# Performance work log

Measured on AMD Instinct MI355X. Metric: run time of the kernel, lower is better.

The kernel has to match this reference:

```python
import jax, jax.numpy as jnp
import numpy as np

N = 100000      # nodes
E = 320000      # edges
G = 2048        # graphs
NODE_F, EDGE_F, HID, EDGE_DIM, L = 48, 6, 256, 128, 8


def setup_inputs() -> dict:
    key = jax.random.key(0)
    ks = jax.random.split(key, 16)
    s = 0.05
    return dict(
        x=jax.random.normal(ks[0], (N, NODE_F), jnp.float32),
        edge_attr=jax.random.normal(ks[1], (E, EDGE_F), jnp.float32),
        node_w=jax.random.normal(ks[2], (NODE_F, HID), jnp.float32) * s,
        node_b=jnp.zeros((HID,), jnp.float32),
        edge_w=jax.random.normal(ks[3], (EDGE_F, EDGE_DIM), jnp.float32) * s,
        edge_b=jnp.zeros((EDGE_DIM,), jnp.float32),
        conv_edge_w=jax.random.normal(ks[4], (L, EDGE_DIM, HID), jnp.float32) * s,
        conv_edge_b=jnp.zeros((L, HID), jnp.float32),
        mlp_w1=jax.random.normal(ks[5], (L, HID, HID), jnp.float32) * s,
        mlp_b1=jnp.zeros((L, HID), jnp.float32),
        mlp_w2=jax.random.normal(ks[6], (L, HID, HID), jnp.float32) * s,
        mlp_b2=jnp.zeros((L, HID), jnp.float32),
        eps=jnp.zeros((L,), jnp.float32),  # GINE trainable eps, init 0
        bn_gamma=jnp.ones((L, HID), jnp.float32),
        bn_beta=jnp.zeros((L, HID), jnp.float32),
        att_w1=jax.random.normal(ks[7], (HID, HID // 2), jnp.float32) * s,
        att_b1=jnp.zeros((HID // 2,), jnp.float32),
        att_w2=jax.random.normal(ks[8], (HID // 2, 1), jnp.float32) * s,
        att_b2=jnp.zeros((1,), jnp.float32),
        edge_index=jax.random.randint(ks[9], (2, E), 0, N),
        batch=jnp.sort(jax.random.randint(ks[10], (N,), 0, G)),
        num_graphs=G,
    )


def reference(x, edge_attr, node_w, node_b, edge_w, edge_b, conv_edge_w, conv_edge_b,
              mlp_w1, mlp_b1, mlp_w2, mlp_b2, eps, bn_gamma, bn_beta,
              att_w1, att_b1, att_w2, att_b2, edge_index, batch, num_graphs):
    seg_sum = lambda v, ids, n: jax.ops.segment_sum(v, ids, num_segments=n)
    n_nodes = x.shape[0]
    src, dst = edge_index[0], edge_index[1]  # x_j gathered from src, aggregated at dst

    h = x @ node_w + node_b                      # node embedding [N, HID]
    e = edge_attr @ edge_w + edge_b              # edge embedding [E, EDGE_DIM]
    cnt = jnp.maximum(seg_sum(jnp.ones((n_nodes,), h.dtype), batch, num_graphs), 1.0)

    for i in range(conv_edge_w.shape[0]):
        # GINEConv: msg = ReLU(x_j + Lin(edge_emb)); add-aggregate; MLP((1+eps)x + agg)
        ee = e @ conv_edge_w[i] + conv_edge_b[i]             # [E, HID]
        msg = jax.nn.relu(h[src] + ee)
        agg = seg_sum(msg, dst, n_nodes)
        z = (1.0 + eps[i]) * h + agg
        z = jax.nn.relu(z @ mlp_w1[i] + mlp_b1[i]) @ mlp_w2[i] + mlp_b2[i]
        # BatchNorm1d (batch statistics, biased var, eps=1e-5)
        mu = z.mean(0)
        var = z.var(0)
        z = bn_gamma[i] * (z - mu) * jax.lax.rsqrt(var + 1e-5) + bn_beta[i]
        # PairNorm (per-graph center, then normalize by sqrt(eps + mean sq norm))
        gmean = seg_sum(z, batch, num_graphs) / cnt[:, None]
        z = z - gmean[batch]
        msq = seg_sum(jnp.sum(z * z, axis=-1), batch, num_graphs) / cnt
        z = z * jax.lax.rsqrt(1e-5 + msq)[batch][:, None]
        h = jax.nn.relu(z)

    # pooling: mean + max + attention (exp-score softmax per graph)
    mean_pool = seg_sum(h, batch, num_graphs) / cnt[:, None]
    max_pool = jax.ops.segment_max(h, batch, num_segments=num_graphs)
    max_pool = jnp.where(jnp.isfinite(max_pool), max_pool, 0.0)
    scores = jnp.tanh(h @ att_w1 + att_b1) @ att_w2 + att_b2   # [N, 1]
    w = jnp.exp(scores)
    w = w / (seg_sum(w, batch, num_graphs)[batch] + 1e-8)
    att_pool = seg_sum(h * w, batch, num_graphs)
    return jnp.concatenate([mean_pool, max_pool, att_pool], axis=-1)  # [G, 768]
```

## Files before the change

### kernel.cpp

```cpp
#include <hip/hip_runtime.h>
#include <cstdint>
#include <cstddef>

#define NN 100000
#define EE 320000
#define GG 2048
#define LL 8

#define O_Z    0ull
#define O_ZB   25600000ull
#define O_HB   38400000ull
#define O_S1   51200000ull
#define O_S2   (O_S1 + 524288ull)
#define O_ABUF (O_S2 + 524288ull)
#define O_BBUF (O_ABUF + 256ull)
#define O_CNTI (O_BBUF + 256ull)
#define O_CNTF (O_CNTI + 2048ull)
#define O_SCOR (O_CNTF + 2048ull)
#define O_WEFF (O_SCOR + 100000ull)
#define O_BEFF (O_WEFF + 12288ull)
#define O_DEG  (O_BEFF + 2048ull)
#define O_STRT (O_DEG + 100000ull)
#define O_BSUM (O_STRT + 100000ull)
#define O_CSR  (O_BSUM + 512ull)
#define O_W1P  (O_CSR + 1280000ull)
#define O_W2P  (O_W1P + 262144ull)
#define O_ATP  (O_W2P + 262144ull)
#define O_GST  (O_ATP + 16384ull)
#define O_NWP  (O_GST + 2048ull)

typedef short s16x8 __attribute__((ext_vector_type(8)));
typedef float f32x4 __attribute__((ext_vector_type(4)));

__device__ inline float b2f(unsigned int lo16) {
  union { float f; unsigned int u; } x; x.u = lo16 << 16; return x.f;
}
__device__ inline unsigned short f2b(float f) {
  union { float f; unsigned int u; } x; x.f = f;
  unsigned int r = x.u + 0x7FFFu + ((x.u >> 16) & 1u);
  return (unsigned short)(r >> 16);
}
__device__ inline unsigned short f2b_lo(float v) {
  unsigned short h = f2b(v);
  float hf = b2f((unsigned int)h);
  return f2b(v - hf);
}

__global__ __launch_bounds__(256) void k_zero(float* __restrict__ p, int n) {
  int i = blockIdx.x * 256 + threadIdx.x;
  int stride = gridDim.x * 256;
  for (; i < n; i += stride) p[i] = 0.0f;
}

__global__ __launch_bounds__(256) void k_count(const int* __restrict__ batch, int* __restrict__ cnti, int n) {
  int i = blockIdx.x * 256 + threadIdx.x;
  if (i < n) atomicAdd(&cnti[batch[i]], 1);
}

__global__ __launch_bounds__(256) void k_gscan(const int* __restrict__ cnti, int* __restrict__ gstart,
                                               float* __restrict__ cntf) {
  __shared__ int part[256];
  int t = threadIdx.x;
  int base = t * 8;
  int loc[8];
  int s = 0;
#pragma unroll
  for (int i = 0; i < 8; ++i) { loc[i] = s; s += cnti[base + i]; }
  part[t] = s;
  __syncthreads();
  for (int off = 1; off < 256; off <<= 1) {
    int u = (t >= off) ? part[t - off] : 0;
    __syncthreads();
    part[t] += u;
    __syncthreads();
  }
  int p = (t > 0) ? part[t - 1] : 0;
#pragma unroll
  for (int i = 0; i < 8; ++i) {
    gstart[base + i] = p + loc[i];
    float v = (float)cnti[base + i];
    cntf[base + i] = v > 1.0f ? v : 1.0f;
  }
}

__global__ __launch_bounds__(256) void k_deg(const int* __restrict__ edst, int* __restrict__ deg, int ne) {
  int e = blockIdx.x * 256 + threadIdx.x;
  if (e < ne) atomicAdd(&deg[edst[e]], 1);
}

__global__ __launch_bounds__(256) void k_scan_part(const int* __restrict__ deg, int* __restrict__ start,
                                                   int* __restrict__ bsum, int n) {
  __shared__ int s[256];
  int i = blockIdx.x * 256 + threadIdx.x;
  int t = threadIdx.x;
  int v = (i < n) ? deg[i] : 0;
  s[t] = v;
  __syncthreads();
  for (int off = 1; off < 256; off <<= 1) {
    int u = (t >= off) ? s[t - off] : 0;
    __syncthreads();
    s[t] += u;
    __syncthreads();
  }
  if (i < n) start[i] = s[t] - v;
  if (t == 255) bsum[blockIdx.x] = s[255];
}

__global__ __launch_bounds__(512) void k_scan_top(int* __restrict__ bsum, int nb) {
  __shared__ int s[512];
  int t = threadIdx.x;
  int v = (t < nb) ? bsum[t] : 0;
  s[t] = v;
  __syncthreads();
  for (int off = 1; off < 512; off <<= 1) {
    int u = (t >= off) ? s[t - off] : 0;
    __syncthreads();
    s[t] += u;
    __syncthreads();
  }
  if (t < nb) bsum[t] = s[t] - v;
}

__global__ __launch_bounds__(256) void k_scan_add(int* __restrict__ start, const int* __restrict__ bsum,
                                                  int* __restrict__ cursor, int n) {
  int i = blockIdx.x * 256 + threadIdx.x;
  if (i < n) {
    int v = start[i] + bsum[blockIdx.x];
    start[i] = v;
    cursor[i] = v;
  }
}

__global__ __launch_bounds__(256) void k_fill(const float* __restrict__ ea, const int* __restrict__ esrc,
                                              const int* __restrict__ edst, int* __restrict__ cursor,
                                              uint4* __restrict__ csr, int ne) {
  int e = blockIdx.x * 256 + threadIdx.x;
  if (e >= ne) return;
  int d = edst[e];
  int slot = atomicAdd(&cursor[d], 1);
  const float* ap = ea + (size_t)e * 6;
  uint4 v;
  v.x = (unsigned int)f2b(ap[0]) | ((unsigned int)f2b(ap[1]) << 16);
  v.y = (unsigned int)f2b(ap[2]) | ((unsigned int)f2b(ap[3]) << 16);
  v.z = (unsigned int)f2b(ap[4]) | ((unsigned int)f2b(ap[5]) << 16);
  v.w = (unsigned int)esrc[e];
  csr[slot] = v;
}

__global__ __launch_bounds__(256) void k_wfuse(const float* __restrict__ edge_w, const float* __restrict__ edge_b,
                                               const float* __restrict__ conv_w, const float* __restrict__ conv_b,
                                               float* __restrict__ wef, float* __restrict__ bef) {
  __shared__ float ew[6 * 128 + 128];
  int i = blockIdx.x;
  int c = threadIdx.x;
  for (int idx = c; idx < 896; idx += 256)
    ew[idx] = idx < 768 ? edge_w[idx] : edge_b[idx - 768];
  __syncthreads();
  float acc[7] = {0.f, 0.f, 0.f, 0.f, 0.f, 0.f, 0.f};
  const float* cw = conv_w + (size_t)i * 32768 + c;
  for (int j = 0; j < 128; ++j) {
    float w = cw[(size_t)j * 256];
#pragma unroll
    for (int k = 0; k < 6; ++k) acc[k] = fmaf(ew[k * 128 + j], w, acc[k]);
    acc[6] = fmaf(ew[768 + j], w, acc[6]);
  }
#pragma unroll
  for (int k = 0; k < 6; ++k) wef[(size_t)i * 1536 + k * 256 + c] = acc[k];
  bef[(size_t)i * 256 + c] = acc[6] + conv_b[(size_t)i * 256 + c];
}

__global__ __launch_bounds__(256) void k_pack_all(const float* __restrict__ mw1, const float* __restrict__ mw2,
                                                  const float* __restrict__ aw1,
                                                  unsigned short* __restrict__ w1p,
                                                  unsigned short* __restrict__ w2p,
                                                  unsigned short* __restrict__ atp) {
  int id = blockIdx.x * 256 + threadIdx.x;
  int cbu = id >> 12;
  if (cbu >= 33) return;
  int lid = id & 4095;
  int l = lid & 63;
  int ct = (lid >> 6) & 7;
  int ks = (lid >> 9) & 7;
  const float* B;
  unsigned short* Bp;
  int ldb, cb;
  if (cbu < 32) {
    int m = cbu >> 1;
    cb = cbu & 1;
    ldb = 256;
    if (m < 8) { B = mw1 + (size_t)m * 65536; Bp = w1p + (size_t)m * 65536; }
    else       { B = mw2 + (size_t)(m - 8) * 65536; Bp = w2p + (size_t)(m - 8) * 65536; }
  } else {
    B = aw1; Bp = atp; ldb = 128; cb = 0;
  }
  int n = cb * 128 + ct * 16 + (l & 15);
  int k0 = ks * 32 + (l >> 4) * 8;
  unsigned short* dst = Bp + (((size_t)cb << 12) | (size_t)lid) * 8;
#pragma unroll
  for (int j = 0; j < 8; ++j) dst[j] = f2b(B[(size_t)(k0 + j) * ldb + n]);
}

__global__ __launch_bounds__(256) void k_pack_node(const float* __restrict__ w,
                                                   unsigned short* __restrict__ Wp) {
  int id = blockIdx.x * 256 + threadIdx.x;
  if (id >= 3072) return;
  int l = id & 63;
  int t = id >> 6;
  int ct = t & 7;
  int u = t >> 3;
  int ks = u % 3;
  int cb = u / 3;
  int n = cb * 128 + ct * 16 + (l & 15);
  unsigned short* dst = Wp + (size_t)id * 8;
#pragma unroll
  for (int j = 0; j < 8; ++j) {
    int kk = ks * 32 + ((l >> 4) << 3) + j;
    int ksrc = kk < 48 ? kk : kk - 48;
    dst[j] = f2b(w[(size_t)ksrc * 256 + n]);
  }
}

__global__ __launch_bounds__(256) void k_embed_mfma(const float* __restrict__ x,
                                                    const unsigned short* __restrict__ Wp,
                                                    const float* __restrict__ b,
                                                    unsigned short* __restrict__ hb, int M) {
  int l = threadIdx.x & 63;
  int w = threadIdx.x >> 6;
  int mloc = l & 15, q = l >> 4;
  int row0 = blockIdx.x * 64 + (w & 1) * 32;
  int colh = (w >> 1) * 128;

  f32x4 acc[2][8];
#pragma unroll
  for (int rt = 0; rt < 2; ++rt)
#pragma unroll
    for (int ct = 0; ct < 8; ++ct) acc[rt][ct] = (f32x4){0.f, 0.f, 0.f, 0.f};

  union { s16x8 v; unsigned short u[8]; } a[2][3];
#pragma unroll
  for (int rt = 0; rt < 2; ++rt) {
    int r = row0 + rt * 16 + mloc;
    if (r > M - 1) r = M - 1;
    const float* xr = x + (size_t)r * 48;
    const float* p0 = xr + q * 8;
    const float* p1 = xr + (q < 2 ? 32 + q * 8 : (q - 2) * 8);
    const float* p2 = xr + 16 + q * 8;
#pragma unroll
    for (int j = 0; j < 8; ++j) {
      a[rt][0].u[j] = f2b(p0[j]);
      a[rt][1].u[j] = (q < 2) ? f2b(p1[j]) : f2b_lo(p1[j]);
      a[rt][2].u[j] = f2b_lo(p2[j]);
    }
  }

  const unsigned short* bp = Wp + (size_t)(colh >> 7) * 12288 + (size_t)l * 8;
#pragma unroll
  for (int ks = 0; ks < 3; ++ks) {
#pragma unroll
    for (int ct = 0; ct < 8; ++ct) {
      s16x8 bb = *(const s16x8*)(bp + ks * 4096 + ct * 512);
      acc[0][ct] = __builtin_amdgcn_mfma_f32_16x16x32_bf16(a[0][ks].v, bb, acc[0][ct], 0, 0, 0);
      acc[1][ct] = __builtin_amdgcn_mfma_f32_16x16x32_bf16(a[1][ks].v, bb, acc[1][ct], 0, 0, 0);
    }
  }

#pragma unroll
  for (int ct = 0; ct < 8; ++ct) {
    int col = colh + ct * 16 + mloc;
    float bv = b[col];
#pragma unroll
    for (int rt = 0; rt < 2; ++rt)
#pragma unroll
      for (int r = 0; r < 4; ++r) {
        int row = row0 + rt * 16 + q * 4 + r;
        if (row < M) hb[(size_t)row * 256 + col] = f2b(acc[rt][ct][r] + bv);
      }
  }
}

__global__ __launch_bounds__(256) void k_edge_csr(const uint4* __restrict__ csr,
                                                  const int* __restrict__ startv, const int* __restrict__ degv,
                                                  const float* __restrict__ wef, const float* __restrict__ bef,
                                                  const unsigned short* __restrict__ hb,
                                                  unsigned short* __restrict__ zb,
                                                  const float* __restrict__ eps, int layer, int n) {
  int lane = threadIdx.x & 63;
  int wv = threadIdx.x >> 6;
  int v0 = (blockIdx.x * 4 + wv) * 4;
  if (v0 >= n) return;
  int c0 = lane * 4;
  float4 w0 = *(const float4*)(wef + 0 * 256 + c0);
  float4 w1 = *(const float4*)(wef + 1 * 256 + c0);
  float4 w2 = *(const float4*)(wef + 2 * 256 + c0);
  float4 w3 = *(const float4*)(wef + 3 * 256 + c0);
  float4 w4 = *(const float4*)(wef + 4 * 256 + c0);
  float4 w5 = *(const float4*)(wef + 5 * 256 + c0);
  float4 bf = *(const float4*)(bef + c0);
  float s = 1.0f + eps[layer];

  int dg[4], pp[4];
  float4 acc[4];
#pragma unroll
  for (int k = 0; k < 4; ++k) {
    int v = v0 + k;
    dg[k] = degv[v];
    int st = startv[v];
    pp[k] = st < (EE - 1) ? st : (EE - 1);
    uint2 hu = *(const uint2*)(hb + (size_t)v * 256 + c0);
    acc[k].x = s * b2f(hu.x & 0xFFFFu);
    acc[k].y = s * b2f(hu.x >> 16);
    acc[k].z = s * b2f(hu.y & 0xFFFFu);
    acc[k].w = s * b2f(hu.y >> 16);
  }
  int mx = dg[0] > dg[1] ? dg[0] : dg[1];
  int mx2 = dg[2] > dg[3] ? dg[2] : dg[3];
  if (mx2 > mx) mx = mx2;

  for (int t = 0; t < mx; ++t) {
    uint4 e[4];
#pragma unroll
    for (int k = 0; k < 4; ++k) e[k] = csr[pp[k]];
    uint2 g[4];
#pragma unroll
    for (int k = 0; k < 4; ++k) g[k] = *(const uint2*)(hb + (size_t)(int)e[k].w * 256 + c0);
#pragma unroll
    for (int k = 0; k < 4; ++k) {
      if (t < dg[k]) {
        float a0 = b2f(e[k].x & 0xFFFFu), a1 = b2f(e[k].x >> 16), a2 = b2f(e[k].y & 0xFFFFu);
        float a3 = b2f(e[k].y >> 16), a4 = b2f(e[k].z & 0xFFFFu), a5 = b2f(e[k].z >> 16);
        float mxv = fmaf(a0, w0.x, fmaf(a1, w1.x, fmaf(a2, w2.x, fmaf(a3, w3.x, fmaf(a4, w4.x, fmaf(a5, w5.x, b2f(g[k].x & 0xFFFFu) + bf.x))))));
        float myv = fmaf(a0, w0.y, fmaf(a1, w1.y, fmaf(a2, w2.y, fmaf(a3, w3.y, fmaf(a4, w4.y, fmaf(a5, w5.y, b2f(g[k].x >> 16) + bf.y))))));
        float mzv = fmaf(a0, w0.z, fmaf(a1, w1.z, fmaf(a2, w2.z, fmaf(a3, w3.z, fmaf(a4, w4.z, fmaf(a5, w5.z, b2f(g[k].y & 0xFFFFu) + bf.z))))));
        float mwv = fmaf(a0, w0.w, fmaf(a1, w1.w, fmaf(a2, w2.w, fmaf(a3, w3.w, fmaf(a4, w4.w, fmaf(a5, w5.w, b2f(g[k].y >> 16) + bf.w))))));
        acc[k].x += mxv > 0.f ? mxv : 0.f;
        acc[k].y += myv > 0.f ? myv : 0.f;
        acc[k].z += mzv > 0.f ? mzv : 0.f;
        acc[k].w += mwv > 0.f ? mwv : 0.f;
      }
      pp[k] += (t < dg[k] - 1) ? 1 : 0;
    }
  }
#pragma unroll
  for (int k = 0; k < 4; ++k) {
    uint2 o;
    o.x = (unsigned int)f2b(acc[k].x) | ((unsigned int)f2b(acc[k].y) << 16);
    o.y = (unsigned int)f2b(acc[k].z) | ((unsigned int)f2b(acc[k].w) << 16);
    *(uint2*)(zb + (size_t)(v0 + k) * 256 + c0) = o;
  }
}

__global__ __launch_bounds__(256, 4) void k_mlp(const unsigned short* __restrict__ A,
                                                const unsigned short* __restrict__ W1p,
                                                const float* __restrict__ b1,
                                                const unsigned short* __restrict__ W2p,
                                                const float* __restrict__ b2,
                                                float* __restrict__ Z,
                                                const int* __restrict__ batchv,
                                                float* __restrict__ S1, float* __restrict__ S2, int M) {
  __shared__ __align__(16) unsigned char smem[33024];
  unsigned short* t1s = (unsigned short*)smem;
  float* zc = (float*)smem;
  int l = threadIdx.x & 63;
  int w = threadIdx.x >> 6;
  int mloc = l & 15, q = l >> 4;
  int rowg = (w & 1) * 32;
  int colh = (w >> 1) * 128;
  int row0 = blockIdx.x * 64;

  const unsigned short* ap[2];
#pragma unroll
  for (int rt = 0; rt < 2; ++rt) {
    int r = row0 + rowg + rt * 16 + mloc;
    if (r > M - 1) r = M - 1;
    ap[rt] = A + (size_t)r * 256 + q * 8;
  }
  f32x4 acc[2][8];
#pragma unroll
  for (int rt = 0; rt < 2; ++rt)
#pragma unroll
    for (int ct = 0; ct < 8; ++ct) acc[rt][ct] = (f32x4){0.f, 0.f, 0.f, 0.f};

  const unsigned short* w1base = W1p + ((size_t)(colh >> 7)) * 32768 + (size_t)l * 8;
#pragma unroll
  for (int ks = 0; ks < 8; ++ks) {
    s16x8 a0 = *(const s16x8*)(ap[0] + ks * 32);
    s16x8 a1 = *(const s16x8*)(ap[1] + ks * 32);
#pragma unroll
    for (int ct = 0; ct < 8; ++ct) {
      s16x8 b = *(const s16x8*)(w1base + ks * 4096 + ct * 512);
      acc[0][ct] = __builtin_amdgcn_mfma_f32_16x16x32_bf16(a0, b, acc[0][ct], 0, 0, 0);
      acc[1][ct] = __builtin_amdgcn_mfma_f32_16x16x32_bf16(a1, b, acc[1][ct], 0, 0, 0);
    }
  }
#pragma unroll
  for (int ct = 0; ct < 8; ++ct) {
    int col = colh + ct * 16 + mloc;
    float bv = b1[col];
    int cc = col >> 3, pos = col & 7;
#pragma unroll
    for (int rt = 0; rt < 2; ++rt)
#pragma unroll
      for (int r = 0; r < 4; ++r) {
        int row = rowg + rt * 16 + q * 4 + r;
        float v = acc[rt][ct][r] + bv;
        v = v > 0.f ? v : 0.f;
        t1s[row * 256 + ((cc ^ (row & 31)) << 3) + pos] = f2b(v);
      }
  }
  __syncthreads();
#pragma unroll
  for (int rt = 0; rt < 2; ++rt)
#pragma unroll
    for (int ct = 0; ct < 8; ++ct) acc[rt][ct] = (f32x4){0.f, 0.f, 0.f, 0.f};
  const unsigned short* w2base = W2p + ((size_t)(colh >> 7)) * 32768 + (size_t)l * 8;
#pragma unroll
  for (int ks = 0; ks < 8; ++ks) {
    s16x8 a[2];
#pragma unroll
    for (int rt = 0; rt < 2; ++rt) {
      int row = rowg + rt * 16 + mloc;
      int cc = (q + ks * 4) ^ (row & 31);
      a[rt] = *(const s16x8*)(t1s + row * 256 + (cc << 3));
    }
#pragma unroll
    for (int ct = 0; ct < 8; ++ct) {
      s16x8 b = *(const s16x8*)(w2base + ks * 4096 + ct * 512);
      acc[0][ct] = __builtin_amdgcn_mfma_f32_16x16x32_bf16(a[0], b, acc[0][ct], 0, 0, 0);
      acc[1][ct] = __builtin_amdgcn_mfma_f32_16x16x32_bf16(a[1], b, acc[1][ct], 0, 0, 0);
    }
  }
  float bv2[8];
#pragma unroll
  for (int ct = 0; ct < 8; ++ct) bv2[ct] = b2[colh + ct * 16 + mloc];

#pragma unroll
  for (int half = 0; half < 2; ++half) {
    __syncthreads();
    if ((w & 1) == half) {
#pragma unroll
      for (int ct = 0; ct < 8; ++ct) {
        int col = colh + ct * 16 + mloc;
#pragma unroll
        for (int rt = 0; rt < 2; ++rt)
#pragma unroll
          for (int r = 0; r < 4; ++r) {
            int row = rt * 16 + q * 4 + r;
            zc[row * 258 + col] = acc[rt][ct][r] + bv2[ct];
          }
      }
    }
    __syncthreads();
    int baserow = row0 + half * 32;
#pragma unroll
    for (int it = 0; it < 8; ++it) {
      int row = it * 4 + w;
      int grow = baserow + row;
      float4 vv = *(const float4*)(zc + row * 258 + l * 4);
      if (grow < M) *(float4*)(Z + (size_t)grow * 256 + l * 4) = vv;
    }
    {
      int c = threadIdx.x;
      int rend = (M - baserow) < 32 ? (M - baserow) : 32;
      if (rend > 0) {
        float s1 = 0.f, s2 = 0.f;
        int gcur = batchv[baserow];
        for (int row = 0; row < rend; ++row) {
          int g = batchv[baserow + row];
          if (g != gcur) {
            atomicAdd(&S1[(size_t)gcur * 256 + c], s1);
            atomicAdd(&S2[(size_t)gcur * 256 + c], s2);
            s1 = 0.f; s2 = 0.f; gcur = g;
          }
          float v = zc[row * 258 + c];
          s1 += v;
          s2 = fmaf(v, v, s2);
        }
        atomicAdd(&S1[(size_t)gcur * 256 + c], s1);
        atomicAdd(&S2[(size_t)gcur * 256 + c], s2);
      }
    }
  }
}

__global__ __launch_bounds__(256) void k_att(const unsigned short* __restrict__ A,
                                             const unsigned short* __restrict__ Bp,
                                             const float* __restrict__ b1,
                                             const float* __restrict__ w2,
                                             const float* __restrict__ b2,
                                             float* __restrict__ scores, int M) {
  int l = threadIdx.x & 63;
  int w = threadIdx.x >> 6;
  int mloc = l & 15, q = l >> 4;
  int row0 = blockIdx.x * 128 + w * 32;

  int r0 = row0 + mloc;      if (r0 > M - 1) r0 = M - 1;
  int r1 = row0 + 16 + mloc; if (r1 > M - 1) r1 = M - 1;
  const unsigned short* ap0 = A + (size_t)r0 * 256 + q * 8;
  const unsigned short* ap1 = A + (size_t)r1 * 256 + q * 8;
  const unsigned short* bp = Bp + (size_t)l * 8;

  f32x4 acc[2][8];
#pragma unroll
  for (int rt = 0; rt < 2; ++rt)
#pragma unroll
    for (int ct = 0; ct < 8; ++ct) acc[rt][ct] = (f32x4){0.f, 0.f, 0.f, 0.f};
#pragma unroll
  for (int ks = 0; ks < 8; ++ks) {
    s16x8 a0 = *(const s16x8*)(ap0 + ks * 32);
    s16x8 a1 = *(const s16x8*)(ap1 + ks * 32);
#pragma unroll
    for (int ct = 0; ct < 8; ++ct) {
      s16x8 b = *(const s16x8*)(bp + ks * 4096 + ct * 512);
      acc[0][ct] = __builtin_amdgcn_mfma_f32_16x16x32_bf16(a0, b, acc[0][ct], 0, 0, 0);
      acc[1][ct] = __builtin_amdgcn_mfma_f32_16x16x32_bf16(a1, b, acc[1][ct], 0, 0, 0);
    }
  }
  float bv[8], wv[8];
#pragma unroll
  for (int ct = 0; ct < 8; ++ct) {
    bv[ct] = b1[ct * 16 + mloc];
    wv[ct] = w2[ct * 16 + mloc];
  }
  float b2v = b2[0];
#pragma unroll
  for (int rt = 0; rt < 2; ++rt)
#pragma unroll
    for (int r = 0; r < 4; ++r) {
      float p = 0.0f;
#pragma unroll
      for (int ct = 0; ct < 8; ++ct) p = fmaf(tanhf(acc[rt][ct][r] + bv[ct]), wv[ct], p);
      p += __shfl_xor(p, 1, 64);
      p += __shfl_xor(p, 2, 64);
      p += __shfl_xor(p, 4, 64);
      p += __shfl_xor(p, 8, 64);
      int row = row0 + rt * 16 + q * 4 + r;
      if (mloc == 0 && row < M) scores[row] = p + b2v;
    }
}

__global__ __launch_bounds__(256) void k_bn_fin(const float* __restrict__ S1, const float* __restrict__ S2,
                                                const float* __restrict__ gamma, const float* __restrict__ beta,
                                                float* __restrict__ abuf, float* __restrict__ bbuf, int n) {
  __shared__ float r1[256], r2[256];
  int c = blockIdx.x;
  int t = threadIdx.x;
  float s1 = 0.0f, s2 = 0.0f;
  for (int g = t; g < GG; g += 256) {
    s1 += S1[(size_t)g * 256 + c];
    s2 += S2[(size_t)g * 256 + c];
  }
  r1[t] = s1; r2[t] = s2;
  __syncthreads();
  for (int off = 128; off; off >>= 1) {
    if (t < off) { r1[t] += r1[t + off]; r2[t] += r2[t + off]; }
    __syncthreads();
  }
  if (t == 0) {
    float inv = 1.0f / (float)n;
    float mu = r1[0] * inv;
    float var = r2[0] * inv - mu * mu;
    float rstd = rsqrtf(var + 1e-5f);
    float a = gamma[c] * rstd;
    abuf[c] = a;
    bbuf[c] = beta[c] - mu * a;
  }
}

template <int LAST>
__global__ __launch_bounds__(256) void k_apply(float* __restrict__ z, const float* __restrict__ abuf,
                                               const float* __restrict__ bbuf, const int* __restrict__ gstart,
                                               const int* __restrict__ cnti, const float* __restrict__ cntf,
                                               float* __restrict__ S1, float* __restrict__ S2,
                                               unsigned short* __restrict__ hb) {
  __shared__ float rT[256], rM[256];
  int g = blockIdx.x, c = threadIdx.x;
  float a = abuf[c], b = bbuf[c];
  size_t idx = (size_t)g * 256 + c;
  float s1 = S1[idx];
  float s2 = S2[idx];
  S1[idx] = 0.0f;
  S2[idx] = 0.0f;
  float nr = (float)cnti[g];
  float ic = 1.0f / cntf[g];
  float mean = (a * s1 + nr * b) * ic;
  float term = fmaf(a * a, s2, fmaf(2.0f * a * b, s1, nr * b * b));
  rT[c] = term;
  rM[c] = mean * mean;
  __syncthreads();
  for (int off = 128; off; off >>= 1) {
    if (c < off) { rT[c] += rT[c + off]; rM[c] += rM[c + off]; }
    __syncthreads();
  }
  float cr = nr > 0.0f ? 1.0f : 0.0f;
  float rinv = rsqrtf(1e-5f + rT[0] * ic - cr * rM[0]);
  int r0 = gstart[g], r1 = r0 + cnti[g];
  for (int r = r0; r < r1; ++r) {
    float v = (fmaf(a, z[(size_t)r * 256 + c], b) - mean) * rinv;
    v = v > 0.0f ? v : 0.0f;
    hb[(size_t)r * 256 + c] = f2b(v);
    if (LAST) z[(size_t)r * 256 + c] = v;
  }
}

__global__ __launch_bounds__(256) void k_poolout(const float* __restrict__ h, const float* __restrict__ scores,
                                                 const int* __restrict__ gstart, const int* __restrict__ cnti,
                                                 const float* __restrict__ cntf, float* __restrict__ out) {
  int g = blockIdx.x, c = threadIdx.x;
  int r0 = gstart[g], r1 = r0 + cnti[g];
  float ma = 0.0f, aa = 0.0f, mx = 0.0f, wa = 0.0f;
  for (int r = r0; r < r1; ++r) {
    float wgt = __expf(scores[r]);
    float hv = h[(size_t)r * 256 + c];
    ma += hv;
    aa = fmaf(hv, wgt, aa);
    mx = fmaxf(mx, hv);
    wa += wgt;
  }
  out[(size_t)g * 768 + c] = ma / cntf[g];
  out[(size_t)g * 768 + 256 + c] = mx;
  out[(size_t)g * 768 + 512 + c] = aa / (wa + 1e-8f);
}

extern "C" void kernel_launch(void* const* d_in, const int* in_sizes, int n_in,
                              void* d_out, int out_size, void* d_ws, size_t ws_size,
                              hipStream_t stream) {
  const float* x         = (const float*)d_in[0];
  const float* edge_attr = (const float*)d_in[1];
  const float* node_w    = (const float*)d_in[2];
  const float* node_b    = (const float*)d_in[3];
  const float* edge_w    = (const float*)d_in[4];
  const float* edge_b    = (const float*)d_in[5];
  const float* conv_w    = (const float*)d_in[6];
  const float* conv_b    = (const float*)d_in[7];
  const float* mlp_w1    = (const float*)d_in[8];
  const float* mlp_b1    = (const float*)d_in[9];
  const float* mlp_w2    = (const float*)d_in[10];
  const float* mlp_b2    = (const float*)d_in[11];
  const float* eps       = (const float*)d_in[12];
  const float* bn_gamma  = (const float*)d_in[13];
  const float* bn_beta   = (const float*)d_in[14];
  const float* att_w1    = (const float*)d_in[15];
  const float* att_b1    = (const float*)d_in[16];
  const float* att_w2    = (const float*)d_in[17];
  const float* att_b2    = (const float*)d_in[18];
  const int*   eidx      = (const int*)d_in[19];
  const int*   batch     = (const int*)d_in[20];
  float* out = (float*)d_out;
  float* ws  = (float*)d_ws;

  float*          zbuf = ws + O_Z;
  unsigned short* zb   = (unsigned short*)(ws + O_ZB);
  unsigned short* hb   = (unsigned short*)(ws + O_HB);
  float* S1    = ws + O_S1;
  float* S2    = ws + O_S2;
  float* abuf  = ws + O_ABUF;
  float* bbuf  = ws + O_BBUF;
  int*   cnti  = (int*)(ws + O_CNTI);
  float* cntf  = ws + O_CNTF;
  float* scor  = ws + O_SCOR;
  int*   curs  = (int*)(ws + O_SCOR);
  float* weff  = ws + O_WEFF;
  float* beff  = ws + O_BEFF;
  int*   deg   = (int*)(ws + O_DEG);
  int*   strt  = (int*)(ws + O_STRT);
  int*   bsum  = (int*)(ws + O_BSUM);
  uint4* csr   = (uint4*)(ws + O_CSR);
  unsigned short* w1p = (unsigned short*)(ws + O_W1P);
  unsigned short* w2p = (unsigned short*)(ws + O_W2P);
  unsigned short* atp = (unsigned short*)(ws + O_ATP);
  int*   gst   = (int*)(ws + O_GST);
  unsigned short* nwp = (unsigned short*)(ws + O_NWP);
  const int* esrc = eidx;
  const int* edst = eidx + EE;

  k_zero<<<8, 256, 0, stream>>>((float*)cnti, GG);
  k_count<<<(NN + 255) / 256, 256, 0, stream>>>(batch, cnti, NN);
  k_gscan<<<1, 256, 0, stream>>>(cnti, gst, cntf);

  k_wfuse<<<LL, 256, 0, stream>>>(edge_w, edge_b, conv_w, conv_b, weff, beff);
  k_pack_all<<<528, 256, 0, stream>>>(mlp_w1, mlp_w2, att_w1, w1p, w2p, atp);
  k_pack_node<<<12, 256, 0, stream>>>(node_w, nwp);
  k_embed_mfma<<<(NN + 63) / 64, 256, 0, stream>>>(x, nwp, node_b, hb, NN);

  k_zero<<<1024, 256, 0, stream>>>(S1, 2 * 524288);

  const int nscan = (NN + 255) / 256;
  k_zero<<<256, 256, 0, stream>>>((float*)deg, NN);
  k_deg<<<(EE + 255) / 256, 256, 0, stream>>>(edst, deg, EE);
  k_scan_part<<<nscan, 256, 0, stream>>>(deg, strt, bsum, NN);
  k_scan_top<<<1, 512, 0, stream>>>(bsum, nscan);
  k_scan_add<<<nscan, 256, 0, stream>>>(strt, bsum, curs, NN);
  k_fill<<<(EE + 255) / 256, 256, 0, stream>>>(edge_attr, esrc, edst, curs, csr, EE);

  const int mtiles64  = (NN + 63) / 64;
  const int mtiles128 = (NN + 127) / 128;

  for (int i = 0; i < LL; ++i) {
    k_edge_csr<<<NN / 16, 256, 0, stream>>>(csr, strt, deg, weff + (size_t)i * 1536,
                                            beff + (size_t)i * 256, hb, zb, eps, i, NN);
    k_mlp<<<mtiles64, 256, 0, stream>>>(zb, w1p + (size_t)i * 65536, mlp_b1 + (size_t)i * 256,
                                        w2p + (size_t)i * 65536, mlp_b2 + (size_t)i * 256, zbuf,
                                        batch, S1, S2, NN);
    k_bn_fin<<<256, 256, 0, stream>>>(S1, S2, bn_gamma + (size_t)i * 256, bn_beta + (size_t)i * 256,
                                      abuf, bbuf, NN);
    if (i == LL - 1)
      k_apply<1><<<GG, 256, 0, stream>>>(zbuf, abuf, bbuf, gst, cnti, cntf, S1, S2, hb);
    else
      k_apply<0><<<GG, 256, 0, stream>>>(zbuf, abuf, bbuf, gst, cnti, cntf, S1, S2, hb);
  }

  k_att<<<mtiles128, 256, 0, stream>>>(hb, atp, att_b1, att_w2, att_b2, scor, NN);
  k_poolout<<<GG, 256, 0, stream>>>(zbuf, scor, gst, cnti, cntf, out);
}
```

Before: 1.705 ms.

## Stage embed inputs in LDS, prefetch CSR entries, split BN reduction

The node-embedding kernel now loads its 64x48 input tile into shared memory with coalesced loads, so threads no longer read strided rows from global memory. The edge aggregation loop prefetches the next CSR entry while the current neighbor gather is in flight, which shortens the dependent load chain. The BatchNorm finalize step, which ran 256 blocks each striding across 2048 rows of a single column, becomes a two-stage reduction: 64 blocks read coalesced partial sums and one block combines them. This adds a kernel launch per layer and a small partial buffer in the workspace.

```diff
diff --git a/kernel.cpp b/kernel.cpp
--- a/kernel.cpp
+++ b/kernel.cpp
@@ -28,6 +28,7 @@
 #define O_ATP  (O_W2P + 262144ull)
 #define O_GST  (O_ATP + 16384ull)
 #define O_NWP  (O_GST + 2048ull)
+#define O_BNP  (O_NWP + 12288ull)
 
 typedef short s16x8 __attribute__((ext_vector_type(8)));
 typedef float f32x4 __attribute__((ext_vector_type(4)));
@@ -224,10 +225,20 @@
                                                     const unsigned short* __restrict__ Wp,
                                                     const float* __restrict__ b,
                                                     unsigned short* __restrict__ hb, int M) {
-  int l = threadIdx.x & 63;
-  int w = threadIdx.x >> 6;
+  __shared__ float xs[64 * 50];
+  int tid = threadIdx.x;
+  int row0g = blockIdx.x * 64;
+  for (int idx = tid; idx < 3072; idx += 256) {
+    int r = idx / 48, c = idx - r * 48;
+    int gr = row0g + r; if (gr > M - 1) gr = M - 1;
+    xs[r * 50 + c] = x[(size_t)gr * 48 + c];
+  }
+  __syncthreads();
+
+  int l = tid & 63;
+  int w = tid >> 6;
   int mloc = l & 15, q = l >> 4;
-  int row0 = blockIdx.x * 64 + (w & 1) * 32;
+  int rowl0 = (w & 1) * 32;
   int colh = (w >> 1) * 128;
 
   f32x4 acc[2][8];
@@ -239,9 +250,7 @@
   union { s16x8 v; unsigned short u[8]; } a[2][3];
 #pragma unroll
   for (int rt = 0; rt < 2; ++rt) {
-    int r = row0 + rt * 16 + mloc;
-    if (r > M - 1) r = M - 1;
-    const float* xr = x + (size_t)r * 48;
+    const float* xr = xs + (rowl0 + rt * 16 + mloc) * 50;
     const float* p0 = xr + q * 8;
     const float* p1 = xr + (q < 2 ? 32 + q * 8 : (q - 2) * 8);
     const float* p2 = xr + 16 + q * 8;
@@ -272,7 +281,7 @@
     for (int rt = 0; rt < 2; ++rt)
 #pragma unroll
       for (int r = 0; r < 4; ++r) {
-        int row = row0 + rt * 16 + q * 4 + r;
+        int row = row0g + rowl0 + rt * 16 + q * 4 + r;
         if (row < M) hb[(size_t)row * 256 + col] = f2b(acc[rt][ct][r] + bv);
       }
   }
@@ -316,13 +325,20 @@
   int mx2 = dg[2] > dg[3] ? dg[2] : dg[3];
   if (mx2 > mx) mx = mx2;
 
+  uint4 e[4];
+#pragma unroll
+  for (int k = 0; k < 4; ++k) e[k] = csr[pp[k]];
+
   for (int t = 0; t < mx; ++t) {
-    uint4 e[4];
-#pragma unroll
-    for (int k = 0; k < 4; ++k) e[k] = csr[pp[k]];
     uint2 g[4];
 #pragma unroll
     for (int k = 0; k < 4; ++k) g[k] = *(const uint2*)(hb + (size_t)(int)e[k].w * 256 + c0);
+    uint4 en[4];
+#pragma unroll
+    for (int k = 0; k < 4; ++k) {
+      pp[k] += (t < dg[k] - 1) ? 1 : 0;
+      en[k] = csr[pp[k]];
+    }
 #pragma unroll
     for (int k = 0; k < 4; ++k) {
       if (t < dg[k]) {
@@ -337,7 +353,7 @@
         acc[k].z += mzv > 0.f ? mzv : 0.f;
         acc[k].w += mwv > 0.f ? mwv : 0.f;
       }
-      pp[k] += (t < dg[k] - 1) ? 1 : 0;
+      e[k] = en[k];
     }
   }
 #pragma unroll
@@ -538,32 +554,34 @@
     }
 }
 
-__global__ __launch_bounds__(256) void k_bn_fin(const float* __restrict__ S1, const float* __restrict__ S2,
-                                                const float* __restrict__ gamma, const float* __restrict__ beta,
-                                                float* __restrict__ abuf, float* __restrict__ bbuf, int n) {
-  __shared__ float r1[256], r2[256];
-  int c = blockIdx.x;
-  int t = threadIdx.x;
+__global__ __launch_bounds__(256) void k_bn_part(const float* __restrict__ S1, const float* __restrict__ S2,
+                                                 float* __restrict__ P1, float* __restrict__ P2) {
+  int b = blockIdx.x, c = threadIdx.x;
   float s1 = 0.0f, s2 = 0.0f;
-  for (int g = t; g < GG; g += 256) {
+  for (int g = b * 32; g < b * 32 + 32; ++g) {
     s1 += S1[(size_t)g * 256 + c];
     s2 += S2[(size_t)g * 256 + c];
   }
-  r1[t] = s1; r2[t] = s2;
-  __syncthreads();
-  for (int off = 128; off; off >>= 1) {
-    if (t < off) { r1[t] += r1[t + off]; r2[t] += r2[t + off]; }
-    __syncthreads();
-  }
-  if (t == 0) {
-    float inv = 1.0f / (float)n;
-    float mu = r1[0] * inv;
-    float var = r2[0] * inv - mu * mu;
-    float rstd = rsqrtf(var + 1e-5f);
-    float a = gamma[c] * rstd;
-    abuf[c] = a;
-    bbuf[c] = beta[c] - mu * a;
-  }
+  P1[(size_t)b * 256 + c] = s1;
+  P2[(size_t)b * 256 + c] = s2;
+}
+
+__global__ __launch_bounds__(256) void k_bn_fin2(const float* __restrict__ P1, const float* __restrict__ P2,
+                                                 const float* __restrict__ gamma, const float* __restrict__ beta,
+                                                 float* __restrict__ abuf, float* __restrict__ bbuf, int n) {
+  int c = threadIdx.x;
+  float s1 = 0.0f, s2 = 0.0f;
+  for (int r = 0; r < 64; ++r) {
+    s1 += P1[(size_t)r * 256 + c];
+    s2 += P2[(size_t)r * 256 + c];
+  }
+  float inv = 1.0f / (float)n;
+  float mu = s1 * inv;
+  float var = s2 * inv - mu * mu;
+  float rstd = rsqrtf(var + 1e-5f);
+  float a = gamma[c] * rstd;
+  abuf[c] = a;
+  bbuf[c] = beta[c] - mu * a;
 }
 
 template <int LAST>
@@ -670,6 +688,8 @@
   unsigned short* atp = (unsigned short*)(ws + O_ATP);
   int*   gst   = (int*)(ws + O_GST);
   unsigned short* nwp = (unsigned short*)(ws + O_NWP);
+  float* bnp1  = ws + O_BNP;
+  float* bnp2  = ws + O_BNP + 16384;
   const int* esrc = eidx;
   const int* edst = eidx + EE;
 
@@ -701,8 +721,9 @@
     k_mlp<<<mtiles64, 256, 0, stream>>>(zb, w1p + (size_t)i * 65536, mlp_b1 + (size_t)i * 256,
                                         w2p + (size_t)i * 65536, mlp_b2 + (size_t)i * 256, zbuf,
                                         batch, S1, S2, NN);
-    k_bn_fin<<<256, 256, 0, stream>>>(S1, S2, bn_gamma + (size_t)i * 256, bn_beta + (size_t)i * 256,
-                                      abuf, bbuf, NN);
+    k_bn_part<<<64, 256, 0, stream>>>(S1, S2, bnp1, bnp2);
+    k_bn_fin2<<<1, 256, 0, stream>>>(bnp1, bnp2, bn_gamma + (size_t)i * 256,
+                                     bn_beta + (size_t)i * 256, abuf, bbuf, NN);
     if (i == LL - 1)
       k_apply<1><<<GG, 256, 0, stream>>>(zbuf, abuf, bbuf, gst, cnti, cntf, S1, S2, hb);
     else
```

Result: faster. 1.560 ms, median of 2 (-8.5%).
